# Performance work log

Hardware: AMD Instinct MI355X
Metric: run time of the kernel (lower is better)

The kernel has to match this reference:

```python
import jax, jax.numpy as jnp
import numpy as np

def mexican_hat(z):
    z2 = z * z
    return (1.0 - z2) * jnp.exp(-0.5 * z2)

def setup_inputs() -> dict:
    key = jax.random.key(0)
    k1, k2 = jax.random.split(key)
    B, N, D = 8192, 512, 64
    x = jax.random.normal(k1, (B, D), dtype=jnp.float32)
    centers = jax.random.normal(k2, (N, D), dtype=jnp.float32)
    scales = jnp.ones((N, D), dtype=jnp.float32)
    return {"x": x, "centers": centers, "scales": scales}

def reference(x, centers, scales):
    # x: (B, D); centers/scales: (N, D)
    z = (x[:, None, :] - centers[None, :, :]) / scales[None, :, :]  # (B, N, D)
    psi = mexican_hat(z)
    h = jnp.prod(psi, axis=2)  # (B, N)
    return h
```

## Files before the change

kernel.cpp:

```cpp
#include <hip/hip_runtime.h>


#define DD 64
#define BSTRIP 8

typedef float v2f __attribute__((ext_vector_type(2)));

__global__ __launch_bounds__(256)
void prep(const float* __restrict__ c, const float* __restrict__ s,
          float4* __restrict__ pp, int N) {
    int i = blockIdx.x * 256 + threadIdx.x;
    if (i < (DD / 2) * N) {
        int dp = i / N, n = i - dp * N;
        float r0 = 1.0f / s[n * DD + 2 * dp];
        float r1 = 1.0f / s[n * DD + 2 * dp + 1];
        pp[i] = make_float4(c[n * DD + 2 * dp] * r0,
                            c[n * DD + 2 * dp + 1] * r1, r0, r1);
    }
}

__global__ __launch_bounds__(256, 2)
void wavelet_kernel(const float* __restrict__ x,
                    const float4* __restrict__ pp,
                    float* __restrict__ out, int B, int N) {
    __shared__ float xls[32][DD];

    int t = threadIdx.x;
    int lane = t & 63;
    int wv = __builtin_amdgcn_readfirstlane(t >> 6);
    int n0 = blockIdx.y * 64;
    int n = n0 + lane;
    int bblk = blockIdx.x * 32;

    {
        const float4* xg = (const float4*)(x + (size_t)bblk * DD);
        float4* xl = (float4*)&xls[0][0];
        xl[t] = xg[t];
        xl[t + 256] = xg[t + 256];
    }
    __syncthreads();

    const float4* pcol = pp + n;

    float acc[BSTRIP];
#pragma unroll
    for (int bi = 0; bi < BSTRIP; ++bi) acc[bi] = 1.0f;

#pragma unroll
    for (int h = 0; h < 4; ++h) {
        v2f cp[8], rs[8];
#pragma unroll
        for (int i = 0; i < 8; ++i) {
            float4 q = pcol[(size_t)(h * 8 + i) * N];
            cp[i] = (v2f){q.x, q.y};
            rs[i] = (v2f){q.z, q.w};
        }

#pragma unroll
        for (int bi = 0; bi < BSTRIP; ++bi) {
            const float4* xq = (const float4*)&xls[wv * BSTRIP + bi][h * 16];
            float4 X0 = xq[0];
            float4 X1 = xq[1];
            float4 X2 = xq[2];
            float4 X3 = xq[3];
            float xs[16] = {X0.x, X0.y, X0.z, X0.w,
                            X1.x, X1.y, X1.z, X1.w,
                            X2.x, X2.y, X2.z, X2.w,
                            X3.x, X3.y, X3.z, X3.w};
            v2f p  = {1.0f, 1.0f};
            v2f s2 = {0.0f, 0.0f};
#pragma unroll
            for (int k = 0; k < 8; ++k) {
                v2f xv = {xs[2 * k], xs[2 * k + 1]};
                v2f z = __builtin_elementwise_fma(xv, rs[k], -cp[k]);
                v2f w = z * z;
                p = __builtin_elementwise_fma(-w, p, p);
                s2 += w;
            }
            acc[bi] *= (p.x * p.y) *
                       __builtin_exp2f(-0.72134752f * (s2.x + s2.y));
        }
    }

#pragma unroll
    for (int bi = 0; bi < BSTRIP; ++bi)
        out[(size_t)(bblk + wv * BSTRIP + bi) * N + n] = acc[bi];
}

extern "C" void kernel_launch(void* const* d_in, const int* in_sizes, int n_in,
                              void* d_out, int out_size, void* d_ws, size_t ws_size,
                              hipStream_t stream) {
    const float* x = (const float*)d_in[0];
    const float* c = (const float*)d_in[1];
    const float* s = (const float*)d_in[2];
    float* out = (float*)d_out;

    int B = in_sizes[0] / DD;
    int N = in_sizes[1] / DD;

    float4* pp = (float4*)d_ws;

    int total = (DD / 2) * N;
    prep<<<(total + 255) / 256, 256, 0, stream>>>(c, s, pp, N);

    dim3 grid(B / 32, N / 64);
    wavelet_kernel<<<grid, 256, 0, stream>>>(x, pp, out, B, N);
}
```

Before: 86.75 us.

## Keep x rows in registers, broadcast center params, stage output through LDS

Restructures the mapping so each lane holds one x row (64 floats) in registers and each wave loops over 16 centers, reading center/inv-scale-squared pairs as wave-uniform loads. The z computation is reformulated as (x-c)^2 * (1/s^2), with a simpler prep kernel. Results go through a padded LDS tile so global stores are coalesced float4 rows. This trades the old vectorized v2f math and per-thread center registers for high register pressure (64-element xr) and scalar, non-packed arithmetic.

```diff
diff --git a/kernel.cpp b/kernel.cpp
--- a/kernel.cpp
+++ b/kernel.cpp
@@ -2,89 +2,81 @@
 
 
 #define DD 64
-#define BSTRIP 8
-
-typedef float v2f __attribute__((ext_vector_type(2)));
 
 __global__ __launch_bounds__(256)
 void prep(const float* __restrict__ c, const float* __restrict__ s,
-          float4* __restrict__ pp, int N) {
+          float2* __restrict__ pq, int total) {
     int i = blockIdx.x * 256 + threadIdx.x;
-    if (i < (DD / 2) * N) {
-        int dp = i / N, n = i - dp * N;
-        float r0 = 1.0f / s[n * DD + 2 * dp];
-        float r1 = 1.0f / s[n * DD + 2 * dp + 1];
-        pp[i] = make_float4(c[n * DD + 2 * dp] * r0,
-                            c[n * DD + 2 * dp + 1] * r1, r0, r1);
+    if (i < total) {
+        float sv = s[i];
+        pq[i] = make_float2(c[i], 1.0f / (sv * sv));
     }
 }
 
 __global__ __launch_bounds__(256, 2)
 void wavelet_kernel(const float* __restrict__ x,
-                    const float4* __restrict__ pp,
+                    const float2* __restrict__ pq,
                     float* __restrict__ out, int B, int N) {
-    __shared__ float xls[32][DD];
+    __shared__ float xs[64 * 65];
+    __shared__ float ol[64 * 65];
 
     int t = threadIdx.x;
     int lane = t & 63;
     int wv = __builtin_amdgcn_readfirstlane(t >> 6);
-    int n0 = blockIdx.y * 64;
-    int n = n0 + lane;
-    int bblk = blockIdx.x * 32;
+    int bblk = blockIdx.x * 64;
+    int nblk = blockIdx.y * 64;
 
     {
         const float4* xg = (const float4*)(x + (size_t)bblk * DD);
-        float4* xl = (float4*)&xls[0][0];
-        xl[t] = xg[t];
-        xl[t + 256] = xg[t + 256];
+#pragma unroll
+        for (int j = 0; j < 4; ++j) {
+            int idx = j * 256 + t;
+            int row = idx >> 4, c4 = idx & 15;
+            float4 v = xg[idx];
+            float* p = &xs[row * 65 + c4 * 4];
+            p[0] = v.x; p[1] = v.y; p[2] = v.z; p[3] = v.w;
+        }
     }
     __syncthreads();
 
-    const float4* pcol = pp + n;
+    float xr[DD];
+#pragma unroll
+    for (int d = 0; d < DD; ++d) xr[d] = xs[lane * 65 + d];
 
-    float acc[BSTRIP];
+#pragma unroll 1
+    for (int ni = 0; ni < 16; ++ni) {
+        int n = nblk + wv * 16 + ni;
+        const float2* P = pq + (size_t)n * DD;
+        float acc = 1.0f;
 #pragma unroll
-    for (int bi = 0; bi < BSTRIP; ++bi) acc[bi] = 1.0f;
+        for (int k = 0; k < 4; ++k) {
+            float p = 1.0f, s2 = 0.0f;
+#pragma unroll
+            for (int i = 0; i < 16; ++i) {
+                float2 q = P[k * 16 + i];
+                float tt = xr[k * 16 + i] - q.x;
+                float w  = tt * tt;
+                float wr = w * q.y;
+                p = __builtin_fmaf(-wr, p, p);
+                s2 += wr;
+            }
+            acc *= p * __builtin_exp2f(-0.72134752f * s2);
+        }
+        ol[lane * 65 + wv * 16 + ni] = acc;
+    }
+    __syncthreads();
 
+    {
+        int row = t >> 2, seg = t & 3;
+        float* orow = out + (size_t)(bblk + row) * N + nblk + seg * 16;
+        const float* l = &ol[row * 65 + seg * 16];
 #pragma unroll
-    for (int h = 0; h < 4; ++h) {
-        v2f cp[8], rs[8];
-#pragma unroll
-        for (int i = 0; i < 8; ++i) {
-            float4 q = pcol[(size_t)(h * 8 + i) * N];
-            cp[i] = (v2f){q.x, q.y};
-            rs[i] = (v2f){q.z, q.w};
-        }
-
-#pragma unroll
-        for (int bi = 0; bi < BSTRIP; ++bi) {
-            const float4* xq = (const float4*)&xls[wv * BSTRIP + bi][h * 16];
-            float4 X0 = xq[0];
-            float4 X1 = xq[1];
-            float4 X2 = xq[2];
-            float4 X3 = xq[3];
-            float xs[16] = {X0.x, X0.y, X0.z, X0.w,
-                            X1.x, X1.y, X1.z, X1.w,
-                            X2.x, X2.y, X2.z, X2.w,
-                            X3.x, X3.y, X3.z, X3.w};
-            v2f p  = {1.0f, 1.0f};
-            v2f s2 = {0.0f, 0.0f};
-#pragma unroll
-            for (int k = 0; k < 8; ++k) {
-                v2f xv = {xs[2 * k], xs[2 * k + 1]};
-                v2f z = __builtin_elementwise_fma(xv, rs[k], -cp[k]);
-                v2f w = z * z;
-                p = __builtin_elementwise_fma(-w, p, p);
-                s2 += w;
-            }
-            acc[bi] *= (p.x * p.y) *
-                       __builtin_exp2f(-0.72134752f * (s2.x + s2.y));
+        for (int j4 = 0; j4 < 4; ++j4) {
+            float4 v = make_float4(l[j4 * 4], l[j4 * 4 + 1],
+                                   l[j4 * 4 + 2], l[j4 * 4 + 3]);
+            ((float4*)orow)[j4] = v;
         }
     }
-
-#pragma unroll
-    for (int bi = 0; bi < BSTRIP; ++bi)
-        out[(size_t)(bblk + wv * BSTRIP + bi) * N + n] = acc[bi];
 }
 
 extern "C" void kernel_launch(void* const* d_in, const int* in_sizes, int n_in,
@@ -98,11 +90,11 @@
     int B = in_sizes[0] / DD;
     int N = in_sizes[1] / DD;
 
-    float4* pp = (float4*)d_ws;
+    float2* pq = (float2*)d_ws;
 
-    int total = (DD / 2) * N;
-    prep<<<(total + 255) / 256, 256, 0, stream>>>(c, s, pp, N);
+    int total = N * DD;
+    prep<<<(total + 255) / 256, 256, 0, stream>>>(c, s, pq, total);
 
-    dim3 grid(B / 32, N / 64);
-    wavelet_kernel<<<grid, 256, 0, stream>>>(x, pp, out, B, N);
+    dim3 grid(B / 64, N / 64);
+    wavelet_kernel<<<grid, 256, 0, stream>>>(x, pq, out, B, N);
 }
```

New measurement: 120.2 us. +38.5%, slower.
